# Performance work log

Measured on AMD Instinct MI355X. Metric: run time of the kernel, lower is better.

The kernel has to match this reference:

```python
import jax, jax.numpy as jnp
import numpy as np

B, S, D = 4, 4096, 1024          # batch, seq, d_model
K, H, A = 32, 4, 2               # mem_key_dim, mem_hashes, mem_assoc
T, NB = 65536, 16                # mem_buckets = 2**NB
Dm, Tv = 64, 32                  # mem_dim, mem_vsa_dim
READ_TEMP, VSA_W = 1.0, 1.0
TANH_SCALE, BETA, NOV_THR = 1.0, 1.0, 0.0
WRITE_THR, ETA = 0.5, 0.1


def setup_inputs() -> dict:
    key = jax.random.key(0)
    k = jax.random.split(key, 12)
    s = 0.02
    return {
        "u": jax.random.normal(k[0], (B, S, D), jnp.float32),
        "Wq": jax.random.normal(k[1], (K, D), jnp.float32) * s,
        "Ww": jax.random.normal(k[2], (K, D), jnp.float32) * s,
        "Wv": jax.random.normal(k[3], (Dm, D), jnp.float32) * s,
        "Wout": jax.random.normal(k[4], (D, Dm), jnp.float32) * s,
        "Wg": jax.random.normal(k[5], (1, D), jnp.float32) * s,
        "bg": jnp.zeros((1,), jnp.float32),
        "R": jax.random.normal(k[6], (H, K, NB), jnp.float32),
        "P": jax.random.normal(k[7], (Tv, K), jnp.float32) / np.float32(np.sqrt(K)),
        "mem_keys": jax.random.normal(k[8], (T, A, K), jnp.float32),
        "mem_vals": jax.random.normal(k[9], (T, A, Dm), jnp.float32),
        "mem_tags": jnp.tanh(jax.random.normal(k[10], (T, A, Tv), jnp.float32)),
    }


def reference(u, Wq, Ww, Wv, Wout, Wg, bg, R, P, mem_keys, mem_vals, mem_tags):
    # --- routing (BitRouter): sign bits of random projections -> bucket per hash ---
    q = jnp.einsum('bsd,kd->bsk', u, Wq)                              # query tag
    bits = (jnp.einsum('bsk,hkn->bshn', q, R) > 0).astype(jnp.int32)
    pw = 2 ** jnp.arange(NB, dtype=jnp.int32)
    idx = jnp.sum(bits * pw, axis=-1)                                 # [B,S,H] in [0,T)

    # --- read: gather bucket slots, key + VSA-tag scores, softmax over H*A ---
    Kg, Vg, Tg = mem_keys[idx], mem_vals[idx], mem_tags[idx]          # [B,S,H,A,*]
    score = jnp.einsum('bsk,bshak->bsha', q, Kg) / jnp.sqrt(jnp.float32(K))
    qt = jnp.tanh(TANH_SCALE * jnp.einsum('bsk,tk->bst', q, P))       # VSA tag of query
    score = score + VSA_W * jnp.einsum('bst,bshat->bsha', qt, Tg) / Tv
    attn = jax.nn.softmax((score / READ_TEMP).reshape(B, S, H * A), axis=-1)
    attn = attn.reshape(B, S, H, A)
    read = jnp.einsum('bsha,bshad->bsd', attn, Vg)                    # [B,S,Dm]
    y = jnp.einsum('bsm,dm->bsd', read, Wout)                         # [B,S,D]

    # --- write: gate + VSA novelty, blend best-matching slot, scatter-add ---
    wk = jnp.einsum('bsd,kd->bsk', u, Ww)
    v = jnp.einsum('bsd,md->bsm', u, Wv)
    g = jax.nn.sigmoid(jnp.einsum('bsd,od->bso', u, Wg) + bg)[..., 0]  # [B,S]
    wt = jnp.tanh(TANH_SCALE * jnp.einsum('bsk,tk->bst', wk, P))
    match = jnp.einsum('bst,bshat->bsha', wt, Tg) / Tv
    slot = jnp.argmax(match, axis=-1)                                  # [B,S,H]
    nov = jax.nn.sigmoid(BETA * (NOV_THR - jnp.max(match, axis=-1)))   # novelty gate
    w = ETA * (g * (g > WRITE_THR))[..., None] * nov                   # [B,S,H]
    flat = (idx * A + slot).reshape(-1)                                # [B*S*H]

    def blend(table, gathered, target, dim):
        cur = jnp.take_along_axis(gathered, slot[..., None, None], axis=3)[..., 0, :]
        d = (w[..., None] * (target[:, :, None, :] - cur)).reshape(-1, dim)
        return table.reshape(T * A, dim).at[flat].add(d).reshape(T, A, dim)

    new_keys = blend(mem_keys, Kg, wk, K)
    new_vals = blend(mem_vals, Vg, v, Dm)
    new_tags = blend(mem_tags, Tg, wt, Tv)
    return y, new_keys, new_vals, new_tags
```

## Files before the change

### kernel.cpp

```cpp
#include <hip/hip_runtime.h>
#include <hip/hip_bf16.h>
#include <cstdint>

#define BB 4
#define SS 4096
#define DD 1024
#define KK 32
#define HH 4
#define AA 2
#define TT 65536
#define NBB 16
#define DM 64
#define TV 32
#define MTOK (BB*SS)
#define PKS 4
#define PKL (DD/PKS)

#define WAVE_FENCE() asm volatile("s_waitcnt lgkmcnt(0)" ::: "memory")

__global__ __launch_bounds__(256) void copy_kernel(
    const float* __restrict__ mem_keys, const float* __restrict__ mem_vals,
    const float* __restrict__ mem_tags, float* __restrict__ tab_o)
{
    const size_t NK = (size_t)TT * AA * KK;
    const size_t NV = (size_t)TT * AA * DM;
    const size_t NT = (size_t)TT * AA * TV;
    const size_t total4 = (NK + NV + NT) / 4;
    size_t i = (size_t)blockIdx.x * 256 + threadIdx.x;
    const size_t stride = (size_t)gridDim.x * 256;
    for (; i < total4; i += stride) {
        size_t e = i * 4;
        float4 val;
        if (e < NK)           val = *(const float4*)(mem_keys + e);
        else if (e < NK + NV) val = *(const float4*)(mem_vals + (e - NK));
        else                  val = *(const float4*)(mem_tags + (e - NK - NV));
        *(float4*)(tab_o + e) = val;
    }
}

__global__ __launch_bounds__(256, 2) void proj_kernel(
    const float* __restrict__ u, const float* __restrict__ Wq,
    const float* __restrict__ Ww, const float* __restrict__ Wv,
    const float* __restrict__ Wg,
    float* __restrict__ qs, float* __restrict__ wks,
    float* __restrict__ vs, float* __restrict__ gs)
{
    __shared__ float u_t[128][36];
    __shared__ float w_t[128][36];
    const int t  = threadIdx.x;
    const int mb = blockIdx.x & 127;
    const int ks = blockIdx.x >> 7;
    const int m0 = mb * 128;
    const int kb = ks * PKL;
    const int r0 = t >> 3;
    const int c8 = t & 7;
    const int ty = t >> 4;
    const int tx = t & 15;

    float acc[8][8];
#pragma unroll
    for (int i = 0; i < 8; i++)
#pragma unroll
        for (int j = 0; j < 8; j++) acc[i][j] = 0.f;
    float gp[4] = {0.f, 0.f, 0.f, 0.f};

    float4 ur[4], wr[4], wg4;
    {
        int kc = kb;
#pragma unroll
        for (int p = 0; p < 4; p++)
            ur[p] = *(const float4*)(u + (size_t)(m0 + r0 + 32 * p) * DD + kc + c8 * 4);
#pragma unroll
        for (int p = 0; p < 4; p++) {
            int c = r0 + 32 * p;
            const float* wrow = (c < 32)  ? (Wq + (size_t)c * DD)
                              : (c < 64)  ? (Ww + (size_t)(c - 32) * DD)
                                          : (Wv + (size_t)(c - 64) * DD);
            wr[p] = *(const float4*)(wrow + kc + c8 * 4);
        }
        wg4 = *(const float4*)(Wg + kc + c8 * 4);
    }

    for (int it = 0; it < 8; ++it) {
        if (it) __syncthreads();
#pragma unroll
        for (int p = 0; p < 4; p++) {
            int r = r0 + 32 * p;
            *(float4*)&u_t[r][c8 * 4] = ur[p];
            gp[p] = fmaf(ur[p].x, wg4.x, fmaf(ur[p].y, wg4.y,
                     fmaf(ur[p].z, wg4.z, fmaf(ur[p].w, wg4.w, gp[p]))));
            *(float4*)&w_t[r][c8 * 4] = wr[p];
        }
        if (it < 7) {
            int kc = kb + (it + 1) * 32;
#pragma unroll
            for (int p = 0; p < 4; p++)
                ur[p] = *(const float4*)(u + (size_t)(m0 + r0 + 32 * p) * DD + kc + c8 * 4);
#pragma unroll
            for (int p = 0; p < 4; p++) {
                int c = r0 + 32 * p;
                const float* wrow = (c < 32)  ? (Wq + (size_t)c * DD)
                                  : (c < 64)  ? (Ww + (size_t)(c - 32) * DD)
                                              : (Wv + (size_t)(c - 64) * DD);
                wr[p] = *(const float4*)(wrow + kc + c8 * 4);
            }
            wg4 = *(const float4*)(Wg + kc + c8 * 4);
        }
        __syncthreads();
#pragma unroll
        for (int k4 = 0; k4 < 8; k4++) {
            float4 a4[8], b4[8];
#pragma unroll
            for (int i = 0; i < 8; i++) a4[i] = *(const float4*)&u_t[ty + 16 * i][k4 * 4];
#pragma unroll
            for (int j = 0; j < 8; j++) b4[j] = *(const float4*)&w_t[tx + 16 * j][k4 * 4];
#pragma unroll
            for (int i = 0; i < 8; i++)
#pragma unroll
                for (int j = 0; j < 8; j++) {
                    acc[i][j] = fmaf(a4[i].x, b4[j].x, acc[i][j]);
                    acc[i][j] = fmaf(a4[i].y, b4[j].y, acc[i][j]);
                    acc[i][j] = fmaf(a4[i].z, b4[j].z, acc[i][j]);
                    acc[i][j] = fmaf(a4[i].w, b4[j].w, acc[i][j]);
                }
        }
    }
#pragma unroll
    for (int p = 0; p < 4; p++) {
        gp[p] += __shfl_xor(gp[p], 1);
        gp[p] += __shfl_xor(gp[p], 2);
        gp[p] += __shfl_xor(gp[p], 4);
    }
    if (c8 == 0) {
#pragma unroll
        for (int p = 0; p < 4; p++) gs[(size_t)ks * MTOK + m0 + r0 + 32 * p] = gp[p];
    }
#pragma unroll
    for (int i = 0; i < 8; i++) {
        int row = m0 + ty + 16 * i;
#pragma unroll
        for (int j = 0; j < 8; j++) {
            if (j < 2)      qs[(size_t)ks * MTOK * KK + (size_t)row * KK + tx + 16 * j]        = acc[i][j];
            else if (j < 4) wks[(size_t)ks * MTOK * KK + (size_t)row * KK + tx + 16 * (j - 2)] = acc[i][j];
            else            vs[(size_t)ks * MTOK * DM + (size_t)row * DM + tx + 16 * (j - 4)]  = acc[i][j];
        }
    }
}

__global__ __launch_bounds__(256) void route_kernel(
    const float* __restrict__ R, const float* __restrict__ P,
    const float* __restrict__ mem_keys, const float* __restrict__ mem_vals,
    const float* __restrict__ mem_tags, const float* __restrict__ bg,
    const float* __restrict__ qs, const float* __restrict__ wks,
    const float* __restrict__ vsl, const float* __restrict__ gsl,
    float* __restrict__ read_o,
    float* __restrict__ keys_o, float* __restrict__ vals_o, float* __restrict__ tags_o)
{
    __shared__ float R_s[4 * 528];
    __shared__ float P_s[TV][KK + 1];
    __shared__ float q_s[4][KK], wk_s[4][KK], qt_s[4][TV], wt_s[4][TV];
    __shared__ float kg_s[4][8][KK], tg_s[4][8][TV], vg_s[4][8][DM];
    __shared__ float sc_s[4][8], mt_s[4][8];
    __shared__ float w_s[4][HH];
    __shared__ int   idx_s[4][HH], slot_s[4][HH];

    const int t    = threadIdx.x;
    const int wid  = t >> 6;
    const int lane = t & 63;

    for (int e = t; e < 2048; e += 256) R_s[(e >> 9) * 528 + (e & 511)] = R[e];
    for (int e = t; e < TV * KK; e += 256) P_s[e >> 5][e & 31] = P[e];
    const float bgv = bg[0];

    float qw[4];
    {
        const int l2 = lane & 31;
        const float* src = (lane < 32) ? qs : wks;
#pragma unroll
        for (int ti = 0; ti < 4; ti++) {
            const int tok = blockIdx.x * 16 + wid * 4 + ti;
            float s = 0.f;
#pragma unroll
            for (int sl = 0; sl < PKS; sl++) s += src[(size_t)sl * MTOK * KK + (size_t)tok * KK + l2];
            qw[ti] = s;
        }
    }
    __syncthreads();

    for (int ti = 0; ti < 4; ti++) {
        const int tok = blockIdx.x * 16 + wid * 4 + ti;
        if (lane < 32) q_s[wid][lane] = qw[ti];
        else           wk_s[wid][lane - 32] = qw[ti];
        float vsum = 0.f;
#pragma unroll
        for (int sl = 0; sl < PKS; sl++) vsum += vsl[(size_t)sl * MTOK * DM + (size_t)tok * DM + lane];
        WAVE_FENCE();
        {
            int h = lane >> 4, n = lane & 15;
            float s = 0.f;
#pragma unroll
            for (int k = 0; k < KK; k++) s = fmaf(q_s[wid][k], R_s[h * 528 + k * 16 + n], s);
            unsigned long long m = __ballot(s > 0.f);
            if (n == 0) idx_s[wid][h] = (int)((m >> (h * 16)) & 0xFFFFull);
        }
        if (lane < 32) {
            float s = 0.f;
#pragma unroll
            for (int k = 0; k < KK; k++) s = fmaf(q_s[wid][k], P_s[lane][k], s);
            qt_s[wid][lane] = tanhf(s);
        } else {
            int t2 = lane - 32;
            float s = 0.f;
#pragma unroll
            for (int k = 0; k < KK; k++) s = fmaf(wk_s[wid][k], P_s[t2][k], s);
            wt_s[wid][t2] = tanhf(s);
        }
        WAVE_FENCE();
        {
            int p = lane >> 3, j = lane & 7;
            int h = p >> 1, a = p & 1;
            size_t sb = (size_t)idx_s[wid][h] * AA + a;
            *(float4*)&kg_s[wid][p][j * 4] = *(const float4*)(mem_keys + sb * KK + j * 4);
            *(float4*)&tg_s[wid][p][j * 4] = *(const float4*)(mem_tags + sb * TV + j * 4);
            *(float4*)&vg_s[wid][p][j * 8]     = *(const float4*)(mem_vals + sb * DM + j * 8);
            *(float4*)&vg_s[wid][p][j * 8 + 4] = *(const float4*)(mem_vals + sb * DM + j * 8 + 4);
        }
        WAVE_FENCE();
        if (lane < 8) {
            int p = lane;
            float s1 = 0.f, s2 = 0.f;
#pragma unroll
            for (int k = 0; k < KK; k++) s1 = fmaf(q_s[wid][k], kg_s[wid][p][k], s1);
#pragma unroll
            for (int k = 0; k < TV; k++) s2 = fmaf(qt_s[wid][k], tg_s[wid][p][k], s2);
            sc_s[wid][p] = s1 * 0.17677669529663688f + s2 * (1.0f / 32.0f);
        } else if (lane < 16) {
            int p = lane - 8;
            float s2 = 0.f;
#pragma unroll
            for (int k = 0; k < TV; k++) s2 = fmaf(wt_s[wid][k], tg_s[wid][p][k], s2);
            mt_s[wid][p] = s2 * (1.0f / 32.0f);
        }
        WAVE_FENCE();
        {
            float sc[8];
#pragma unroll
            for (int p = 0; p < 8; p++) sc[p] = sc_s[wid][p];
            float mx = sc[0];
#pragma unroll
            for (int p = 1; p < 8; p++) mx = fmaxf(mx, sc[p]);
            float e[8], den = 0.f;
#pragma unroll
            for (int p = 0; p < 8; p++) { e[p] = expf(sc[p] - mx); den += e[p]; }
            float inv = 1.f / den;
            float r = 0.f;
#pragma unroll
            for (int p = 0; p < 8; p++) r = fmaf(e[p] * inv, vg_s[wid][p][lane], r);
            read_o[(size_t)tok * DM + lane] = r;
        }
        if (lane < HH) {
            int h = lane;
            float m0v = mt_s[wid][h * 2], m1v = mt_s[wid][h * 2 + 1];
            int sl = (m1v > m0v) ? 1 : 0;
            float mm = fmaxf(m0v, m1v);
            float nov = 1.f / (1.f + expf(mm));
            float gd = bgv;
#pragma unroll
            for (int s2 = 0; s2 < PKS; s2++) gd += gsl[(size_t)s2 * MTOK + tok];
            float gg = 1.f / (1.f + expf(-gd));
            float wv = (gg > 0.5f) ? (0.1f * gg * nov) : 0.f;
            slot_s[wid][h] = sl;
            w_s[wid][h] = wv;
        }
        WAVE_FENCE();
        if (w_s[wid][0] != 0.f) {
            int h = lane >> 4, c = lane & 15;
            float wv = w_s[wid][h];
            int sl8 = slot_s[wid][h];
            size_t flat = (size_t)idx_s[wid][h] * AA + sl8;
            int p = h * 2 + sl8;
#pragma unroll
            for (int m = 0; m < 2; m++) {
                int cc = c + 16 * m;
                atomicAdd(keys_o + flat * KK + cc, wv * (wk_s[wid][cc] - kg_s[wid][p][cc]));
                atomicAdd(tags_o + flat * TV + cc, wv * (wt_s[wid][cc] - tg_s[wid][p][cc]));
            }
#pragma unroll
            for (int m = 0; m < 4; m++) {
                int cc = c + 16 * m;
                float vv = __shfl(vsum, cc);
                atomicAdd(vals_o + flat * DM + cc, wv * (vv - vg_s[wid][p][cc]));
            }
        }
        WAVE_FENCE();
    }
}

__global__ __launch_bounds__(256, 2) void ygemm_kernel(
    const float* __restrict__ read_i, const float* __restrict__ Wout,
    float* __restrict__ y_o)
{
    __shared__ float rd_t[128][36];
    __shared__ float wo_t[128][36];
    const int t  = threadIdx.x;
    const int m0 = blockIdx.x * 128;
    const int n0 = blockIdx.y * 128;
    const int r0 = t >> 3;
    const int c8 = t & 7;
    const int ty = t >> 4;
    const int tx = t & 15;

    float acc[8][8];
#pragma unroll
    for (int i = 0; i < 8; i++)
#pragma unroll
        for (int j = 0; j < 8; j++) acc[i][j] = 0.f;

    float4 rr[4], wwr[4];
#pragma unroll
    for (int p = 0; p < 4; p++) {
        int r = r0 + 32 * p;
        rr[p]  = *(const float4*)(read_i + (size_t)(m0 + r) * DM + c8 * 4);
        wwr[p] = *(const float4*)(Wout  + (size_t)(n0 + r) * DM + c8 * 4);
    }
    for (int it = 0; it < 2; ++it) {
        if (it) __syncthreads();
#pragma unroll
        for (int p = 0; p < 4; p++) {
            int r = r0 + 32 * p;
            *(float4*)&rd_t[r][c8 * 4] = rr[p];
            *(float4*)&wo_t[r][c8 * 4] = wwr[p];
        }
        if (it == 0) {
#pragma unroll
            for (int p = 0; p < 4; p++) {
                int r = r0 + 32 * p;
                rr[p]  = *(const float4*)(read_i + (size_t)(m0 + r) * DM + 32 + c8 * 4);
                wwr[p] = *(const float4*)(Wout  + (size_t)(n0 + r) * DM + 32 + c8 * 4);
            }
        }
        __syncthreads();
#pragma unroll
        for (int k4 = 0; k4 < 8; k4++) {
            float4 a4[8], b4[8];
#pragma unroll
            for (int i = 0; i < 8; i++) a4[i] = *(const float4*)&rd_t[ty + 16 * i][k4 * 4];
#pragma unroll
            for (int j = 0; j < 8; j++) b4[j] = *(const float4*)&wo_t[(j >> 2) * 64 + tx * 4 + (j & 3)][k4 * 4];
#pragma unroll
            for (int i = 0; i < 8; i++)
#pragma unroll
                for (int j = 0; j < 8; j++) {
                    acc[i][j] = fmaf(a4[i].x, b4[j].x, acc[i][j]);
                    acc[i][j] = fmaf(a4[i].y, b4[j].y, acc[i][j]);
                    acc[i][j] = fmaf(a4[i].z, b4[j].z, acc[i][j]);
                    acc[i][j] = fmaf(a4[i].w, b4[j].w, acc[i][j]);
                }
        }
    }
#pragma unroll
    for (int i = 0; i < 8; i++) {
        size_t row = (size_t)(m0 + ty + 16 * i) * DD + n0;
        *(float4*)&y_o[row + tx * 4]      = make_float4(acc[i][0], acc[i][1], acc[i][2], acc[i][3]);
        *(float4*)&y_o[row + 64 + tx * 4] = make_float4(acc[i][4], acc[i][5], acc[i][6], acc[i][7]);
    }
}

extern "C" void kernel_launch(void* const* d_in, const int* in_sizes, int n_in,
                              void* d_out, int out_size, void* d_ws, size_t ws_size,
                              hipStream_t stream)
{
    (void)in_sizes; (void)n_in; (void)out_size; (void)ws_size;
    const float* u    = (const float*)d_in[0];
    const float* Wq   = (const float*)d_in[1];
    const float* Ww   = (const float*)d_in[2];
    const float* Wv   = (const float*)d_in[3];
    const float* Wout = (const float*)d_in[4];
    const float* Wg   = (const float*)d_in[5];
    const float* bg   = (const float*)d_in[6];
    const float* R    = (const float*)d_in[7];
    const float* P    = (const float*)d_in[8];
    const float* mem_keys = (const float*)d_in[9];
    const float* mem_vals = (const float*)d_in[10];
    const float* mem_tags = (const float*)d_in[11];

    float* y_o    = (float*)d_out;
    float* keys_o = y_o    + (size_t)MTOK * DD;
    float* vals_o = keys_o + (size_t)TT * AA * KK;
    float* tags_o = vals_o + (size_t)TT * AA * DM;

    float* qs  = y_o;
    float* wks = qs  + (size_t)PKS * MTOK * KK;
    float* vsl = wks + (size_t)PKS * MTOK * KK;
    float* gsl = vsl + (size_t)PKS * MTOK * DM;

    float* read_w = (float*)d_ws;

    copy_kernel<<<2048, 256, 0, stream>>>(mem_keys, mem_vals, mem_tags, keys_o);
    proj_kernel<<<128 * PKS, 256, 0, stream>>>(u, Wq, Ww, Wv, Wg, qs, wks, vsl, gsl);
    route_kernel<<<MTOK / 16, 256, 0, stream>>>(R, P, mem_keys, mem_vals, mem_tags, bg,
                                                qs, wks, vsl, gsl, read_w,
                                                keys_o, vals_o, tags_o);
    ygemm_kernel<<<dim3(MTOK / 128, DD / 128), 256, 0, stream>>>(read_w, Wout, y_o);
}
```

Measured before the change: 413.3 us.

## Halve proj tile rows for more blocks; simplify ygemm loads and stores

The projection GEMM now uses 64-row token tiles instead of 128, doubling the grid and raising launch bounds to 4 blocks per CU. This is meant to give better occupancy and load balance across CUs, at the cost of reloading the weight tile twice as often. The output GEMM drops its register prefetch in favour of direct global-to-LDS loads. It also switches to strided column mapping, which replaces the float4 output stores with scalar stores that may coalesce less well.

Measured after the change: 606.4 us. 1.47x slower.

```diff
diff --git a/kernel.cpp b/kernel.cpp
--- a/kernel.cpp
+++ b/kernel.cpp
@@ -38,37 +38,37 @@
     }
 }
 
-__global__ __launch_bounds__(256, 2) void proj_kernel(
+__global__ __launch_bounds__(256, 4) void proj_kernel(
     const float* __restrict__ u, const float* __restrict__ Wq,
     const float* __restrict__ Ww, const float* __restrict__ Wv,
     const float* __restrict__ Wg,
     float* __restrict__ qs, float* __restrict__ wks,
     float* __restrict__ vs, float* __restrict__ gs)
 {
-    __shared__ float u_t[128][36];
+    __shared__ float u_t[64][36];
     __shared__ float w_t[128][36];
     const int t  = threadIdx.x;
-    const int mb = blockIdx.x & 127;
-    const int ks = blockIdx.x >> 7;
-    const int m0 = mb * 128;
+    const int mb = blockIdx.x & 255;
+    const int ks = blockIdx.x >> 8;
+    const int m0 = mb * 64;
     const int kb = ks * PKL;
     const int r0 = t >> 3;
     const int c8 = t & 7;
     const int ty = t >> 4;
     const int tx = t & 15;
 
-    float acc[8][8];
-#pragma unroll
-    for (int i = 0; i < 8; i++)
+    float acc[4][8];
+#pragma unroll
+    for (int i = 0; i < 4; i++)
 #pragma unroll
         for (int j = 0; j < 8; j++) acc[i][j] = 0.f;
-    float gp[4] = {0.f, 0.f, 0.f, 0.f};
-
-    float4 ur[4], wr[4], wg4;
+    float gp[2] = {0.f, 0.f};
+
+    float4 ur[2], wr[4], wg4;
     {
         int kc = kb;
 #pragma unroll
-        for (int p = 0; p < 4; p++)
+        for (int p = 0; p < 2; p++)
             ur[p] = *(const float4*)(u + (size_t)(m0 + r0 + 32 * p) * DD + kc + c8 * 4);
 #pragma unroll
         for (int p = 0; p < 4; p++) {
@@ -84,17 +84,19 @@
     for (int it = 0; it < 8; ++it) {
         if (it) __syncthreads();
 #pragma unroll
-        for (int p = 0; p < 4; p++) {
+        for (int p = 0; p < 2; p++) {
             int r = r0 + 32 * p;
             *(float4*)&u_t[r][c8 * 4] = ur[p];
             gp[p] = fmaf(ur[p].x, wg4.x, fmaf(ur[p].y, wg4.y,
                      fmaf(ur[p].z, wg4.z, fmaf(ur[p].w, wg4.w, gp[p]))));
-            *(float4*)&w_t[r][c8 * 4] = wr[p];
-        }
+        }
+#pragma unroll
+        for (int p = 0; p < 4; p++)
+            *(float4*)&w_t[r0 + 32 * p][c8 * 4] = wr[p];
         if (it < 7) {
             int kc = kb + (it + 1) * 32;
 #pragma unroll
-            for (int p = 0; p < 4; p++)
+            for (int p = 0; p < 2; p++)
                 ur[p] = *(const float4*)(u + (size_t)(m0 + r0 + 32 * p) * DD + kc + c8 * 4);
 #pragma unroll
             for (int p = 0; p < 4; p++) {
@@ -109,13 +111,13 @@
         __syncthreads();
 #pragma unroll
         for (int k4 = 0; k4 < 8; k4++) {
-            float4 a4[8], b4[8];
-#pragma unroll
-            for (int i = 0; i < 8; i++) a4[i] = *(const float4*)&u_t[ty + 16 * i][k4 * 4];
+            float4 a4[4], b4[8];
+#pragma unroll
+            for (int i = 0; i < 4; i++) a4[i] = *(const float4*)&u_t[ty + 16 * i][k4 * 4];
 #pragma unroll
             for (int j = 0; j < 8; j++) b4[j] = *(const float4*)&w_t[tx + 16 * j][k4 * 4];
 #pragma unroll
-            for (int i = 0; i < 8; i++)
+            for (int i = 0; i < 4; i++)
 #pragma unroll
                 for (int j = 0; j < 8; j++) {
                     acc[i][j] = fmaf(a4[i].x, b4[j].x, acc[i][j]);
@@ -126,17 +128,17 @@
         }
     }
 #pragma unroll
-    for (int p = 0; p < 4; p++) {
+    for (int p = 0; p < 2; p++) {
         gp[p] += __shfl_xor(gp[p], 1);
         gp[p] += __shfl_xor(gp[p], 2);
         gp[p] += __shfl_xor(gp[p], 4);
     }
     if (c8 == 0) {
 #pragma unroll
-        for (int p = 0; p < 4; p++) gs[(size_t)ks * MTOK + m0 + r0 + 32 * p] = gp[p];
-    }
-#pragma unroll
-    for (int i = 0; i < 8; i++) {
+        for (int p = 0; p < 2; p++) gs[(size_t)ks * MTOK + m0 + r0 + 32 * p] = gp[p];
+    }
+#pragma unroll
+    for (int i = 0; i < 4; i++) {
         int row = m0 + ty + 16 * i;
 #pragma unroll
         for (int j = 0; j < 8; j++) {
@@ -316,28 +318,13 @@
 #pragma unroll
         for (int j = 0; j < 8; j++) acc[i][j] = 0.f;
 
-    float4 rr[4], wwr[4];
-#pragma unroll
-    for (int p = 0; p < 4; p++) {
-        int r = r0 + 32 * p;
-        rr[p]  = *(const float4*)(read_i + (size_t)(m0 + r) * DM + c8 * 4);
-        wwr[p] = *(const float4*)(Wout  + (size_t)(n0 + r) * DM + c8 * 4);
-    }
-    for (int it = 0; it < 2; ++it) {
-        if (it) __syncthreads();
+    for (int k0 = 0; k0 < DM; k0 += 32) {
+        __syncthreads();
 #pragma unroll
         for (int p = 0; p < 4; p++) {
             int r = r0 + 32 * p;
-            *(float4*)&rd_t[r][c8 * 4] = rr[p];
-            *(float4*)&wo_t[r][c8 * 4] = wwr[p];
-        }
-        if (it == 0) {
-#pragma unroll
-            for (int p = 0; p < 4; p++) {
-                int r = r0 + 32 * p;
-                rr[p]  = *(const float4*)(read_i + (size_t)(m0 + r) * DM + 32 + c8 * 4);
-                wwr[p] = *(const float4*)(Wout  + (size_t)(n0 + r) * DM + 32 + c8 * 4);
-            }
+            *(float4*)&rd_t[r][c8 * 4] = *(const float4*)(read_i + (size_t)(m0 + r) * DM + k0 + c8 * 4);
+            *(float4*)&wo_t[r][c8 * 4] = *(const float4*)(Wout  + (size_t)(n0 + r) * DM + k0 + c8 * 4);
         }
         __syncthreads();
 #pragma unroll
@@ -346,7 +333,7 @@
 #pragma unroll
             for (int i = 0; i < 8; i++) a4[i] = *(const float4*)&rd_t[ty + 16 * i][k4 * 4];
 #pragma unroll
-            for (int j = 0; j < 8; j++) b4[j] = *(const float4*)&wo_t[(j >> 2) * 64 + tx * 4 + (j & 3)][k4 * 4];
+            for (int j = 0; j < 8; j++) b4[j] = *(const float4*)&wo_t[tx + 16 * j][k4 * 4];
 #pragma unroll
             for (int i = 0; i < 8; i++)
 #pragma unroll
@@ -361,8 +348,8 @@
 #pragma unroll
     for (int i = 0; i < 8; i++) {
         size_t row = (size_t)(m0 + ty + 16 * i) * DD + n0;
-        *(float4*)&y_o[row + tx * 4]      = make_float4(acc[i][0], acc[i][1], acc[i][2], acc[i][3]);
-        *(float4*)&y_o[row + 64 + tx * 4] = make_float4(acc[i][4], acc[i][5], acc[i][6], acc[i][7]);
+#pragma unroll
+        for (int j = 0; j < 8; j++) y_o[row + tx + 16 * j] = acc[i][j];
     }
 }
 
@@ -397,7 +384,7 @@
     float* read_w = (float*)d_ws;
 
     copy_kernel<<<2048, 256, 0, stream>>>(mem_keys, mem_vals, mem_tags, keys_o);
-    proj_kernel<<<128 * PKS, 256, 0, stream>>>(u, Wq, Ww, Wv, Wg, qs, wks, vsl, gsl);
+    proj_kernel<<<256 * PKS, 256, 0, stream>>>(u, Wq, Ww, Wv, Wg, qs, wks, vsl, gsl);
     route_kernel<<<MTOK / 16, 256, 0, stream>>>(R, P, mem_keys, mem_vals, mem_tags, bg,
                                                 qs, wks, vsl, gsl, read_w,
                                                 keys_o, vals_o, tags_o);
```
